# Optimization experiments

Measured on AMD Instinct MI355X. Metric: run time of the kernel, lower is better.

The kernel has to match this reference:

```python
import jax, jax.numpy as jnp
import numpy as np

EMB = 512
SEQ = 128
BATCH = 512
K = 16
ITERS = 3


def squash(x):
    # x: [..., emb]
    sq = jnp.sum(x * x, axis=-1, keepdims=True)
    scale = sq / (1.0 + sq) / jnp.sqrt(sq + 1e-9)
    return x * scale


def setup_inputs() -> dict:
    key = jax.random.key(0)
    k0, k1, k2, k3, k4 = jax.random.split(key, 5)
    low_capsule = jax.random.normal(k0, (BATCH, SEQ, EMB), dtype=jnp.float32)
    valid_his = jax.random.randint(k1, (BATCH, SEQ), 0, 2, dtype=jnp.int32)
    # torch creates B fresh with N(0,1) inside forward; we pass it in for determinism
    B_init = jax.random.normal(k2, (BATCH, K, SEQ), dtype=jnp.float32)
    W_S = jax.random.normal(k3, (EMB, EMB), dtype=jnp.float32) * 0.02  # S Linear (no bias)
    W_L = jax.random.normal(k4, (EMB, EMB), dtype=jnp.float32) * 0.02  # relu-layer Linear
    b_L = jnp.zeros((EMB,), dtype=jnp.float32)
    return {"low_capsule": low_capsule, "B_init": B_init, "W_S": W_S,
            "W_L": W_L, "b_L": b_L, "valid_his": valid_his}


def reference(low_capsule, B_init, W_S, W_L, b_L, valid_his):
    # low_capsule: [b, s, e]; valid_his: [b, s]; B_init: [b, K, s]
    lc_new = jnp.einsum('bse,fe->bsf', low_capsule, W_S)          # S(low_capsule)
    lc_iter = jax.lax.stop_gradient(lc_new)                        # .detach()
    mask = (valid_his != 0)[:, None, :]                            # [b, 1, s]
    # B never receives gradient in torch (non-leaf, requires_grad=False)
    Bc = jax.lax.stop_gradient(B_init)
    U = None
    for i in range(ITERS):
        W = jax.nn.softmax(Bc, axis=1)                             # softmax over K capsules
        W = jnp.where(mask, W, 0.0)                                # zero out invalid positions
        if i + 1 < ITERS:
            Z = jnp.einsum('bks,bse->bke', W, lc_iter)             # routed capsules
            U = squash(Z)
            Bc = Bc + jnp.einsum('bse,bke->bks', lc_iter, U)       # agreement update
        else:
            Z = jnp.einsum('bks,bse->bke', W, lc_new)              # last iter uses grad path
            U = squash(Z)
    # relu_layer=True: Linear + ReLU on [b, K, e]
    U = jax.nn.relu(jnp.einsum('bke,fe->bkf', U, W_L) + b_L)
    return U
```

## Files before the change

### kernel.cpp

```cpp
#include <hip/hip_runtime.h>
#include <hip/hip_bf16.h>

#define BATCH 512
#define SEQ   128
#define EMB   512
#define KCAP  16

typedef __attribute__((ext_vector_type(4))) float f32x4;
typedef __attribute__((ext_vector_type(8))) short s16x8;

__device__ __forceinline__ unsigned short f2bf(float x) {
    union { float f; unsigned int u; } v; v.f = x;
    unsigned int r = v.u + 0x7fff + ((v.u >> 16) & 1);
    return (unsigned short)(r >> 16);
}
__device__ __forceinline__ float bf2f(unsigned short b) {
    union { float f; unsigned int u; } v; v.u = ((unsigned int)b) << 16;
    return v.f;
}
__device__ __forceinline__ void cvt8(const float* f, s16x8& h, s16x8& l) {
    #pragma unroll
    for (int j = 0; j < 8; ++j) {
        unsigned short hb = f2bf(f[j]);
        h[j] = (short)hb;
        l[j] = (short)f2bf(f[j] - bf2f(hb));
    }
}

__device__ __forceinline__ int swz(int row, int chunk) {
    return row * 32 + ((chunk ^ ((row >> 1) & 3)) << 3);
}

template<bool EPI_BIAS_RELU>
__global__ __launch_bounds__(256, 2)
void gemm_mfma(const float* __restrict__ A, const float* __restrict__ B,
               const float* __restrict__ bias, float* __restrict__ C) {
    __shared__ short lsAh[128 * 32], lsAl[128 * 32];
    __shared__ short lsBh[128 * 32], lsBl[128 * 32];

    const int tid  = threadIdx.x;
    const int lane = tid & 63;
    const int w    = tid >> 6;
    const int wm   = (w & 1) * 64;
    const int wn   = (w >> 1) * 64;
    const size_t row0 = (size_t)(blockIdx.x >> 2) * 128;
    const int    col0 = (int)(blockIdx.x & 3) * 128;

    const int srow = tid >> 1;
    const int skh  = tid & 1;
    const int cb   = skh * 2;
    const float* Ap = A + (row0 + srow) * 512 + skh * 16;
    const float* Bp = B + (size_t)(col0 + srow) * 512 + skh * 16;

    f32x4 acc[4][4];
    #pragma unroll
    for (int i = 0; i < 4; ++i)
        #pragma unroll
        for (int j = 0; j < 4; ++j) acc[i][j] = (f32x4){0.f, 0.f, 0.f, 0.f};

    for (int kt = 0; kt < 512; kt += 32) {
        float fa[16], fb[16];
        *(float4*)&fa[0]  = *(const float4*)(Ap + kt);
        *(float4*)&fa[4]  = *(const float4*)(Ap + kt + 4);
        *(float4*)&fa[8]  = *(const float4*)(Ap + kt + 8);
        *(float4*)&fa[12] = *(const float4*)(Ap + kt + 12);
        *(float4*)&fb[0]  = *(const float4*)(Bp + kt);
        *(float4*)&fb[4]  = *(const float4*)(Bp + kt + 4);
        *(float4*)&fb[8]  = *(const float4*)(Bp + kt + 8);
        *(float4*)&fb[12] = *(const float4*)(Bp + kt + 12);

        __syncthreads();
        s16x8 h, l;
        cvt8(fa,     h, l); *(s16x8*)&lsAh[swz(srow, cb)]     = h; *(s16x8*)&lsAl[swz(srow, cb)]     = l;
        cvt8(fa + 8, h, l); *(s16x8*)&lsAh[swz(srow, cb + 1)] = h; *(s16x8*)&lsAl[swz(srow, cb + 1)] = l;
        cvt8(fb,     h, l); *(s16x8*)&lsBh[swz(srow, cb)]     = h; *(s16x8*)&lsBl[swz(srow, cb)]     = l;
        cvt8(fb + 8, h, l); *(s16x8*)&lsBh[swz(srow, cb + 1)] = h; *(s16x8*)&lsBl[swz(srow, cb + 1)] = l;
        __syncthreads();

        s16x8 ah[4], al[4], bh[4], bl[4];
        const int c = lane >> 4;
        #pragma unroll
        for (int mi = 0; mi < 4; ++mi) {
            const int r = wm + mi * 16 + (lane & 15);
            ah[mi] = *(const s16x8*)&lsAh[swz(r, c)];
            al[mi] = *(const s16x8*)&lsAl[swz(r, c)];
        }
        #pragma unroll
        for (int ni = 0; ni < 4; ++ni) {
            const int r = wn + ni * 16 + (lane & 15);
            bh[ni] = *(const s16x8*)&lsBh[swz(r, c)];
            bl[ni] = *(const s16x8*)&lsBl[swz(r, c)];
        }
        #pragma unroll
        for (int mi = 0; mi < 4; ++mi)
            #pragma unroll
            for (int ni = 0; ni < 4; ++ni) {
                acc[mi][ni] = __builtin_amdgcn_mfma_f32_16x16x32_bf16(ah[mi], bh[ni], acc[mi][ni], 0, 0, 0);
                acc[mi][ni] = __builtin_amdgcn_mfma_f32_16x16x32_bf16(al[mi], bh[ni], acc[mi][ni], 0, 0, 0);
                acc[mi][ni] = __builtin_amdgcn_mfma_f32_16x16x32_bf16(ah[mi], bl[ni], acc[mi][ni], 0, 0, 0);
            }
    }

    #pragma unroll
    for (int ni = 0; ni < 4; ++ni) {
        const int gc = col0 + wn + ni * 16 + (lane & 15);
        float bv = 0.f;
        if (EPI_BIAS_RELU) bv = bias[gc];
        #pragma unroll
        for (int mi = 0; mi < 4; ++mi) {
            const size_t gr = row0 + wm + mi * 16 + ((lane >> 4) << 2);
            #pragma unroll
            for (int r = 0; r < 4; ++r) {
                float v = acc[mi][ni][r];
                if (EPI_BIAS_RELU) v = fmaxf(v + bv, 0.f);
                C[(gr + r) * 512 + gc] = v;
            }
        }
    }
}

__device__ __forceinline__ float dot4(const float4 a, const float4 b) {
    return a.x * b.x + a.y * b.y + a.z * b.z + a.w * b.w;
}

__global__ __launch_bounds__(512, 4)
void routing_kernel(const float* __restrict__ lcn, const float* __restrict__ Binit,
                    const int* __restrict__ valid, float* __restrict__ Uout) {
    __shared__ float sBc[KCAP][SEQ];
    __shared__ float sWt[SEQ][KCAP];
    __shared__ float sU[KCAP][EMB];
    __shared__ float smask[SEQ];

    const int b    = blockIdx.x;
    const int tid  = threadIdx.x;
    const int lane = tid & 63;
    const int w    = tid >> 6;
    const int e0   = (tid & 127) * 4;
    const int k0   = (tid >> 7) * 4;
    const float* lcb = lcn + (size_t)b * (SEQ * EMB);

    for (int i = tid; i < KCAP * SEQ; i += 512)
        ((float*)sBc)[i] = Binit[(size_t)b * (KCAP * SEQ) + i];
    if (tid < SEQ) smask[tid] = (valid[b * SEQ + tid] != 0) ? 1.0f : 0.0f;
    __syncthreads();

    for (int it = 0; it < 3; ++it) {
        if (tid < SEQ) {
            const int s = tid;
            float mx = sBc[0][s];
            #pragma unroll
            for (int k = 1; k < KCAP; ++k) mx = fmaxf(mx, sBc[k][s]);
            float ex[KCAP];
            float sum = 0.f;
            #pragma unroll
            for (int k = 0; k < KCAP; ++k) { ex[k] = expf(sBc[k][s] - mx); sum += ex[k]; }
            const float inv = smask[s] / sum;
            #pragma unroll
            for (int k = 0; k < KCAP; ++k) sWt[s][k] = ex[k] * inv;
        }
        __syncthreads();

        float acc[4][4];
        #pragma unroll
        for (int i = 0; i < 4; ++i)
            #pragma unroll
            for (int j = 0; j < 4; ++j) acc[i][j] = 0.f;
        #pragma unroll 4
        for (int s = 0; s < SEQ; ++s) {
            const float4 v  = *(const float4*)(lcb + s * EMB + e0);
            const float4 wv = *(const float4*)&sWt[s][k0];
            const float wa[4] = {wv.x, wv.y, wv.z, wv.w};
            const float va[4] = {v.x, v.y, v.z, v.w};
            #pragma unroll
            for (int ki = 0; ki < 4; ++ki)
                #pragma unroll
                for (int j = 0; j < 4; ++j) acc[ki][j] += wa[ki] * va[j];
        }
        #pragma unroll
        for (int ki = 0; ki < 4; ++ki) {
            float4 r;
            r.x = acc[ki][0]; r.y = acc[ki][1]; r.z = acc[ki][2]; r.w = acc[ki][3];
            *(float4*)&sU[k0 + ki][e0] = r;
        }
        __syncthreads();

        #pragma unroll
        for (int kk = 2 * w; kk <= 2 * w + 1; ++kk) {
            float4 z0 = *(const float4*)&sU[kk][lane * 4];
            float4 z1 = *(const float4*)&sU[kk][256 + lane * 4];
            float p = dot4(z0, z0) + dot4(z1, z1);
            #pragma unroll
            for (int m = 32; m >= 1; m >>= 1) p += __shfl_xor(p, m, 64);
            const float scale = p / (1.0f + p) / sqrtf(p + 1e-9f);
            z0.x *= scale; z0.y *= scale; z0.z *= scale; z0.w *= scale;
            z1.x *= scale; z1.y *= scale; z1.z *= scale; z1.w *= scale;
            *(float4*)&sU[kk][lane * 4] = z0;
            *(float4*)&sU[kk][256 + lane * 4] = z1;
        }
        __syncthreads();

        if (it < 2) {
            const int ka = 2 * w, kb = 2 * w + 1;
            const float4 ua0 = *(const float4*)&sU[ka][lane * 4];
            const float4 ua1 = *(const float4*)&sU[ka][256 + lane * 4];
            const float4 ub0 = *(const float4*)&sU[kb][lane * 4];
            const float4 ub1 = *(const float4*)&sU[kb][256 + lane * 4];
            #pragma unroll 2
            for (int s = 0; s < SEQ; ++s) {
                const float4 l0 = *(const float4*)(lcb + s * EMB + lane * 4);
                const float4 l1 = *(const float4*)(lcb + s * EMB + 256 + lane * 4);
                float pa = dot4(l0, ua0) + dot4(l1, ua1);
                float pb = dot4(l0, ub0) + dot4(l1, ub1);
                #pragma unroll
                for (int m = 32; m >= 1; m >>= 1) {
                    pa += __shfl_xor(pa, m, 64);
                    pb += __shfl_xor(pb, m, 64);
                }
                if (lane == 0) {
                    sBc[ka][s] += pa;
                    sBc[kb][s] += pb;
                }
            }
            __syncthreads();
        }
    }

    for (int i = tid; i < KCAP * EMB; i += 512)
        Uout[(size_t)b * (KCAP * EMB) + i] = ((const float*)sU)[i];
}

extern "C" void kernel_launch(void* const* d_in, const int* in_sizes, int n_in,
                              void* d_out, int out_size, void* d_ws, size_t ws_size,
                              hipStream_t stream) {
    const float* lc    = (const float*)d_in[0];
    const float* Binit = (const float*)d_in[1];
    const float* W_S   = (const float*)d_in[2];
    const float* W_L   = (const float*)d_in[3];
    const float* b_L   = (const float*)d_in[4];
    const int*   valid = (const int*)d_in[5];
    float* out = (float*)d_out;

    const size_t lcn_elems = (size_t)BATCH * SEQ * EMB;
    const size_t u_elems   = (size_t)BATCH * KCAP * EMB;
    if (ws_size < (lcn_elems + u_elems) * sizeof(float)) return;
    float* lcn = (float*)d_ws;
    float* Uws = lcn + lcn_elems;

    gemm_mfma<false><<<2048, 256, 0, stream>>>(lc, W_S, nullptr, lcn);
    routing_kernel<<<BATCH, 512, 0, stream>>>(lcn, Binit, valid, Uws);
    gemm_mfma<true><<<256, 256, 0, stream>>>(Uws, W_L, b_L, out);
}
```

Before: 603.3 us.

## Prepack weights to bf16 hi/lo, stage routing slabs in LDS, bf16 U output

Weights are split into bf16 hi/lo pairs once by a separate pack kernel, so the GEMMs load packed weights instead of converting B every tile. The routing kernel is restructured to stream 16-row slabs of lc through shared memory, fusing the agreement update, softmax and weighted sum in one pass per iteration rather than reading lc from global memory twice. U is written as bf16 and the final GEMM uses a single bf16 A operand with two MFMAs instead of three. This removes redundant global traffic and conversion work, at the cost of lower precision for U in the output layer and extra small launches.

After: 547.1 us. -9.3%, faster.

```diff
diff --git a/kernel.cpp b/kernel.cpp
--- a/kernel.cpp
+++ b/kernel.cpp
@@ -8,6 +8,8 @@
 
 typedef __attribute__((ext_vector_type(4))) float f32x4;
 typedef __attribute__((ext_vector_type(8))) short s16x8;
+typedef __attribute__((ext_vector_type(4))) unsigned short u16x4;
+typedef __attribute__((ext_vector_type(8))) unsigned short u16x8;
 
 __device__ __forceinline__ unsigned short f2bf(float x) {
     union { float f; unsigned int u; } v; v.f = x;
@@ -26,17 +28,36 @@
         l[j] = (short)f2bf(f[j] - bf2f(hb));
     }
 }
+__device__ __forceinline__ float dot4(const float4 a, const float4 b) {
+    return a.x * b.x + a.y * b.y + a.z * b.z + a.w * b.w;
+}
 
 __device__ __forceinline__ int swz(int row, int chunk) {
     return row * 32 + ((chunk ^ ((row >> 1) & 3)) << 3);
 }
 
-template<bool EPI_BIAS_RELU>
+__global__ void cvt_pack(const float* __restrict__ in, unsigned short* __restrict__ out, int nch) {
+    const int c = blockIdx.x * 256 + threadIdx.x;
+    if (c >= nch) return;
+    float f[8];
+    *(float4*)&f[0] = *(const float4*)(in + c * 8);
+    *(float4*)&f[4] = *(const float4*)(in + c * 8 + 4);
+    u16x8 h, l;
+    #pragma unroll
+    for (int j = 0; j < 8; ++j) {
+        unsigned short hb = f2bf(f[j]);
+        h[j] = hb;
+        l[j] = f2bf(f[j] - bf2f(hb));
+    }
+    *(u16x8*)(out + c * 16) = h;
+    *(u16x8*)(out + c * 16 + 8) = l;
+}
+
 __global__ __launch_bounds__(256, 2)
-void gemm_mfma(const float* __restrict__ A, const float* __restrict__ B,
-               const float* __restrict__ bias, float* __restrict__ C) {
+void gemm_f32a(const float* __restrict__ A, const unsigned short* __restrict__ pkB,
+               float* __restrict__ C) {
     __shared__ short lsAh[128 * 32], lsAl[128 * 32];
-    __shared__ short lsBh[128 * 32], lsBl[128 * 32];
+    __shared__ unsigned short lsB[128 * 64];
 
     const int tid  = threadIdx.x;
     const int lane = tid & 63;
@@ -50,7 +71,16 @@
     const int skh  = tid & 1;
     const int cb   = skh * 2;
     const float* Ap = A + (row0 + srow) * 512 + skh * 16;
-    const float* Bp = B + (size_t)(col0 + srow) * 512 + skh * 16;
+
+    int bo[4], so[4];
+    #pragma unroll
+    for (int i = 0; i < 4; ++i) {
+        const int slot = i * 256 + tid;
+        const int br = slot >> 3, s3 = slot & 7;
+        const int cn = s3 ^ (br & 7);
+        bo[i] = (col0 + br) * 1024 + (cn >> 1) * 16 + (cn & 1) * 8;
+        so[i] = slot * 8;
+    }
 
     f32x4 acc[4][4];
     #pragma unroll
@@ -59,26 +89,25 @@
         for (int j = 0; j < 4; ++j) acc[i][j] = (f32x4){0.f, 0.f, 0.f, 0.f};
 
     for (int kt = 0; kt < 512; kt += 32) {
-        float fa[16], fb[16];
+        float fa[16];
         *(float4*)&fa[0]  = *(const float4*)(Ap + kt);
         *(float4*)&fa[4]  = *(const float4*)(Ap + kt + 4);
         *(float4*)&fa[8]  = *(const float4*)(Ap + kt + 8);
         *(float4*)&fa[12] = *(const float4*)(Ap + kt + 12);
-        *(float4*)&fb[0]  = *(const float4*)(Bp + kt);
-        *(float4*)&fb[4]  = *(const float4*)(Bp + kt + 4);
-        *(float4*)&fb[8]  = *(const float4*)(Bp + kt + 8);
-        *(float4*)&fb[12] = *(const float4*)(Bp + kt + 12);
+        u16x8 bq[4];
+        #pragma unroll
+        for (int i = 0; i < 4; ++i) bq[i] = *(const u16x8*)(pkB + bo[i] + kt * 2);
 
         __syncthreads();
         s16x8 h, l;
         cvt8(fa,     h, l); *(s16x8*)&lsAh[swz(srow, cb)]     = h; *(s16x8*)&lsAl[swz(srow, cb)]     = l;
         cvt8(fa + 8, h, l); *(s16x8*)&lsAh[swz(srow, cb + 1)] = h; *(s16x8*)&lsAl[swz(srow, cb + 1)] = l;
-        cvt8(fb,     h, l); *(s16x8*)&lsBh[swz(srow, cb)]     = h; *(s16x8*)&lsBl[swz(srow, cb)]     = l;
-        cvt8(fb + 8, h, l); *(s16x8*)&lsBh[swz(srow, cb + 1)] = h; *(s16x8*)&lsBl[swz(srow, cb + 1)] = l;
-        __syncthreads();
-
-        s16x8 ah[4], al[4], bh[4], bl[4];
+        #pragma unroll
+        for (int i = 0; i < 4; ++i) *(u16x8*)&lsB[so[i]] = bq[i];
+        __syncthreads();
+
         const int c = lane >> 4;
+        s16x8 ah[4], al[4];
         #pragma unroll
         for (int mi = 0; mi < 4; ++mi) {
             const int r = wm + mi * 16 + (lane & 15);
@@ -88,145 +117,229 @@
         #pragma unroll
         for (int ni = 0; ni < 4; ++ni) {
             const int r = wn + ni * 16 + (lane & 15);
-            bh[ni] = *(const s16x8*)&lsBh[swz(r, c)];
-            bl[ni] = *(const s16x8*)&lsBl[swz(r, c)];
-        }
-        #pragma unroll
-        for (int mi = 0; mi < 4; ++mi)
-            #pragma unroll
-            for (int ni = 0; ni < 4; ++ni) {
-                acc[mi][ni] = __builtin_amdgcn_mfma_f32_16x16x32_bf16(ah[mi], bh[ni], acc[mi][ni], 0, 0, 0);
-                acc[mi][ni] = __builtin_amdgcn_mfma_f32_16x16x32_bf16(al[mi], bh[ni], acc[mi][ni], 0, 0, 0);
-                acc[mi][ni] = __builtin_amdgcn_mfma_f32_16x16x32_bf16(ah[mi], bl[ni], acc[mi][ni], 0, 0, 0);
-            }
+            const s16x8 bh = *(const s16x8*)&lsB[r * 64 + (((2 * c)     ^ (r & 7)) << 3)];
+            const s16x8 bl = *(const s16x8*)&lsB[r * 64 + (((2 * c + 1) ^ (r & 7)) << 3)];
+            #pragma unroll
+            for (int mi = 0; mi < 4; ++mi) {
+                acc[mi][ni] = __builtin_amdgcn_mfma_f32_16x16x32_bf16(ah[mi], bh, acc[mi][ni], 0, 0, 0);
+                acc[mi][ni] = __builtin_amdgcn_mfma_f32_16x16x32_bf16(al[mi], bh, acc[mi][ni], 0, 0, 0);
+                acc[mi][ni] = __builtin_amdgcn_mfma_f32_16x16x32_bf16(ah[mi], bl, acc[mi][ni], 0, 0, 0);
+            }
+        }
     }
 
     #pragma unroll
     for (int ni = 0; ni < 4; ++ni) {
         const int gc = col0 + wn + ni * 16 + (lane & 15);
-        float bv = 0.f;
-        if (EPI_BIAS_RELU) bv = bias[gc];
         #pragma unroll
         for (int mi = 0; mi < 4; ++mi) {
             const size_t gr = row0 + wm + mi * 16 + ((lane >> 4) << 2);
             #pragma unroll
-            for (int r = 0; r < 4; ++r) {
-                float v = acc[mi][ni][r];
-                if (EPI_BIAS_RELU) v = fmaxf(v + bv, 0.f);
-                C[(gr + r) * 512 + gc] = v;
-            }
-        }
-    }
-}
-
-__device__ __forceinline__ float dot4(const float4 a, const float4 b) {
-    return a.x * b.x + a.y * b.y + a.z * b.z + a.w * b.w;
-}
-
-__global__ __launch_bounds__(512, 4)
-void routing_kernel(const float* __restrict__ lcn, const float* __restrict__ Binit,
-                    const int* __restrict__ valid, float* __restrict__ Uout) {
-    __shared__ float sBc[KCAP][SEQ];
-    __shared__ float sWt[SEQ][KCAP];
-    __shared__ float sU[KCAP][EMB];
-    __shared__ float smask[SEQ];
-
-    const int b    = blockIdx.x;
+            for (int r = 0; r < 4; ++r) C[(gr + r) * 512 + gc] = acc[mi][ni][r];
+        }
+    }
+}
+
+__global__ __launch_bounds__(256, 2)
+void gemm_bf16a(const unsigned short* __restrict__ A, const unsigned short* __restrict__ pkB,
+                const float* __restrict__ bias, float* __restrict__ C) {
+    __shared__ unsigned short lsA[128 * 32];
+    __shared__ unsigned short lsB[128 * 64];
+
     const int tid  = threadIdx.x;
     const int lane = tid & 63;
     const int w    = tid >> 6;
-    const int e0   = (tid & 127) * 4;
-    const int k0   = (tid >> 7) * 4;
+    const int wm   = (w & 1) * 64;
+    const int wn   = (w >> 1) * 64;
+    const size_t row0 = (size_t)(blockIdx.x >> 2) * 128;
+    const int    col0 = (int)(blockIdx.x & 3) * 128;
+
+    const int srow = tid >> 1;
+    const int skh  = tid & 1;
+    const int cb   = skh * 2;
+    const unsigned short* Up = A + (row0 + srow) * 512 + skh * 16;
+
+    int bo[4], so[4];
+    #pragma unroll
+    for (int i = 0; i < 4; ++i) {
+        const int slot = i * 256 + tid;
+        const int br = slot >> 3, s3 = slot & 7;
+        const int cn = s3 ^ (br & 7);
+        bo[i] = (col0 + br) * 1024 + (cn >> 1) * 16 + (cn & 1) * 8;
+        so[i] = slot * 8;
+    }
+
+    f32x4 acc[4][4];
+    #pragma unroll
+    for (int i = 0; i < 4; ++i)
+        #pragma unroll
+        for (int j = 0; j < 4; ++j) acc[i][j] = (f32x4){0.f, 0.f, 0.f, 0.f};
+
+    for (int kt = 0; kt < 512; kt += 32) {
+        const u16x8 a0 = *(const u16x8*)(Up + kt);
+        const u16x8 a1 = *(const u16x8*)(Up + kt + 8);
+        u16x8 bq[4];
+        #pragma unroll
+        for (int i = 0; i < 4; ++i) bq[i] = *(const u16x8*)(pkB + bo[i] + kt * 2);
+
+        __syncthreads();
+        *(u16x8*)&lsA[swz(srow, cb)]     = a0;
+        *(u16x8*)&lsA[swz(srow, cb + 1)] = a1;
+        #pragma unroll
+        for (int i = 0; i < 4; ++i) *(u16x8*)&lsB[so[i]] = bq[i];
+        __syncthreads();
+
+        const int c = lane >> 4;
+        s16x8 ah[4];
+        #pragma unroll
+        for (int mi = 0; mi < 4; ++mi)
+            ah[mi] = *(const s16x8*)&lsA[swz(wm + mi * 16 + (lane & 15), c)];
+        #pragma unroll
+        for (int ni = 0; ni < 4; ++ni) {
+            const int r = wn + ni * 16 + (lane & 15);
+            const s16x8 bh = *(const s16x8*)&lsB[r * 64 + (((2 * c)     ^ (r & 7)) << 3)];
+            const s16x8 bl = *(const s16x8*)&lsB[r * 64 + (((2 * c + 1) ^ (r & 7)) << 3)];
+            #pragma unroll
+            for (int mi = 0; mi < 4; ++mi) {
+                acc[mi][ni] = __builtin_amdgcn_mfma_f32_16x16x32_bf16(ah[mi], bh, acc[mi][ni], 0, 0, 0);
+                acc[mi][ni] = __builtin_amdgcn_mfma_f32_16x16x32_bf16(ah[mi], bl, acc[mi][ni], 0, 0, 0);
+            }
+        }
+    }
+
+    #pragma unroll
+    for (int ni = 0; ni < 4; ++ni) {
+        const int gc = col0 + wn + ni * 16 + (lane & 15);
+        const float bv = bias[gc];
+        #pragma unroll
+        for (int mi = 0; mi < 4; ++mi) {
+            const size_t gr = row0 + wm + mi * 16 + ((lane >> 4) << 2);
+            #pragma unroll
+            for (int r = 0; r < 4; ++r)
+                C[(gr + r) * 512 + gc] = fmaxf(acc[mi][ni][r] + bv, 0.f);
+        }
+    }
+}
+
+__global__ __launch_bounds__(512, 2)
+void routing_v2(const float* __restrict__ lcn, const float* __restrict__ Binit,
+                const int* __restrict__ valid, unsigned short* __restrict__ Uh) {
+    __shared__ float sBc[KCAP][SEQ];
+    __shared__ float sWt[16][KCAP];
+    __shared__ float sU[KCAP][EMB];
+    __shared__ float sLc[16][EMB];
+    __shared__ float smask[SEQ];
+
+    const int b = blockIdx.x, t = threadIdx.x;
+    const int lane = t & 63, w = t >> 6;
     const float* lcb = lcn + (size_t)b * (SEQ * EMB);
 
-    for (int i = tid; i < KCAP * SEQ; i += 512)
+    for (int i = t; i < KCAP * SEQ; i += 512)
         ((float*)sBc)[i] = Binit[(size_t)b * (KCAP * SEQ) + i];
-    if (tid < SEQ) smask[tid] = (valid[b * SEQ + tid] != 0) ? 1.0f : 0.0f;
+    if (t < SEQ) smask[t] = (valid[b * SEQ + t] != 0) ? 1.0f : 0.0f;
     __syncthreads();
 
+    const int k0 = (t >> 7) * 4;
+    const int e0 = (t & 127) * 4;
+    const int ka = 2 * w, kb = 2 * w + 1;
+
     for (int it = 0; it < 3; ++it) {
-        if (tid < SEQ) {
-            const int s = tid;
-            float mx = sBc[0][s];
-            #pragma unroll
-            for (int k = 1; k < KCAP; ++k) mx = fmaxf(mx, sBc[k][s]);
-            float ex[KCAP];
-            float sum = 0.f;
-            #pragma unroll
-            for (int k = 0; k < KCAP; ++k) { ex[k] = expf(sBc[k][s] - mx); sum += ex[k]; }
-            const float inv = smask[s] / sum;
-            #pragma unroll
-            for (int k = 0; k < KCAP; ++k) sWt[s][k] = ex[k] * inv;
-        }
-        __syncthreads();
-
-        float acc[4][4];
-        #pragma unroll
-        for (int i = 0; i < 4; ++i)
-            #pragma unroll
-            for (int j = 0; j < 4; ++j) acc[i][j] = 0.f;
-        #pragma unroll 4
-        for (int s = 0; s < SEQ; ++s) {
-            const float4 v  = *(const float4*)(lcb + s * EMB + e0);
-            const float4 wv = *(const float4*)&sWt[s][k0];
-            const float wa[4] = {wv.x, wv.y, wv.z, wv.w};
-            const float va[4] = {v.x, v.y, v.z, v.w};
-            #pragma unroll
-            for (int ki = 0; ki < 4; ++ki)
+        float4 ua0, ua1, ub0, ub1;
+        if (it > 0) {
+            ua0 = *(const float4*)&sU[ka][lane * 4];
+            ua1 = *(const float4*)&sU[ka][256 + lane * 4];
+            ub0 = *(const float4*)&sU[kb][lane * 4];
+            ub1 = *(const float4*)&sU[kb][256 + lane * 4];
+        }
+        f32x4 accZ[4];
+        #pragma unroll
+        for (int i = 0; i < 4; ++i) accZ[i] = (f32x4){0.f, 0.f, 0.f, 0.f};
+
+        for (int slab = 0; slab < 8; ++slab) {
+            {
+                const float4* src = (const float4*)(lcb + slab * 16 * EMB);
+                float4* dst = (float4*)sLc;
                 #pragma unroll
-                for (int j = 0; j < 4; ++j) acc[ki][j] += wa[ki] * va[j];
-        }
-        #pragma unroll
-        for (int ki = 0; ki < 4; ++ki) {
-            float4 r;
-            r.x = acc[ki][0]; r.y = acc[ki][1]; r.z = acc[ki][2]; r.w = acc[ki][3];
-            *(float4*)&sU[k0 + ki][e0] = r;
-        }
-        __syncthreads();
-
-        #pragma unroll
-        for (int kk = 2 * w; kk <= 2 * w + 1; ++kk) {
+                for (int j = 0; j < 4; ++j) dst[t + 512 * j] = src[t + 512 * j];
+            }
+            __syncthreads();
+
+            if (it > 0) {
+                #pragma unroll 4
+                for (int s8 = 0; s8 < 16; ++s8) {
+                    const float4 l0 = *(const float4*)&sLc[s8][lane * 4];
+                    const float4 l1 = *(const float4*)&sLc[s8][256 + lane * 4];
+                    float pa = dot4(l0, ua0) + dot4(l1, ua1);
+                    float pb = dot4(l0, ub0) + dot4(l1, ub1);
+                    #pragma unroll
+                    for (int m = 32; m >= 1; m >>= 1) {
+                        pa += __shfl_xor(pa, m, 64);
+                        pb += __shfl_xor(pb, m, 64);
+                    }
+                    if (lane == 0) {
+                        sBc[ka][slab * 16 + s8] += pa;
+                        sBc[kb][slab * 16 + s8] += pb;
+                    }
+                }
+                __syncthreads();
+            }
+
+            if (t < 256) {
+                const int si = t >> 4, k = t & 15, s = slab * 16 + si;
+                const float v = sBc[k][s];
+                float mx = v;
+                #pragma unroll
+                for (int m = 1; m < 16; m <<= 1) mx = fmaxf(mx, __shfl_xor(mx, m, 64));
+                const float ex = expf(v - mx);
+                float sm = ex;
+                #pragma unroll
+                for (int m = 1; m < 16; m <<= 1) sm += __shfl_xor(sm, m, 64);
+                sWt[si][k] = ex * smask[s] / sm;
+            }
+            __syncthreads();
+
+            #pragma unroll 4
+            for (int si = 0; si < 16; ++si) {
+                const float4 wv = *(const float4*)&sWt[si][k0];
+                const float4 v  = *(const float4*)&sLc[si][e0];
+                const f32x4 vv = {v.x, v.y, v.z, v.w};
+                accZ[0] += vv * wv.x;
+                accZ[1] += vv * wv.y;
+                accZ[2] += vv * wv.z;
+                accZ[3] += vv * wv.w;
+            }
+            __syncthreads();
+        }
+
+        #pragma unroll
+        for (int ki = 0; ki < 4; ++ki) *(f32x4*)&sU[k0 + ki][e0] = accZ[ki];
+        __syncthreads();
+
+        #pragma unroll
+        for (int kk = ka; kk <= kb; ++kk) {
             float4 z0 = *(const float4*)&sU[kk][lane * 4];
             float4 z1 = *(const float4*)&sU[kk][256 + lane * 4];
             float p = dot4(z0, z0) + dot4(z1, z1);
             #pragma unroll
             for (int m = 32; m >= 1; m >>= 1) p += __shfl_xor(p, m, 64);
-            const float scale = p / (1.0f + p) / sqrtf(p + 1e-9f);
-            z0.x *= scale; z0.y *= scale; z0.z *= scale; z0.w *= scale;
-            z1.x *= scale; z1.y *= scale; z1.z *= scale; z1.w *= scale;
+            const float sc = p / (1.0f + p) / sqrtf(p + 1e-9f);
+            z0.x *= sc; z0.y *= sc; z0.z *= sc; z0.w *= sc;
+            z1.x *= sc; z1.y *= sc; z1.z *= sc; z1.w *= sc;
             *(float4*)&sU[kk][lane * 4] = z0;
             *(float4*)&sU[kk][256 + lane * 4] = z1;
         }
         __syncthreads();
-
-        if (it < 2) {
-            const int ka = 2 * w, kb = 2 * w + 1;
-            const float4 ua0 = *(const float4*)&sU[ka][lane * 4];
-            const float4 ua1 = *(const float4*)&sU[ka][256 + lane * 4];
-            const float4 ub0 = *(const float4*)&sU[kb][lane * 4];
-            const float4 ub1 = *(const float4*)&sU[kb][256 + lane * 4];
-            #pragma unroll 2
-            for (int s = 0; s < SEQ; ++s) {
-                const float4 l0 = *(const float4*)(lcb + s * EMB + lane * 4);
-                const float4 l1 = *(const float4*)(lcb + s * EMB + 256 + lane * 4);
-                float pa = dot4(l0, ua0) + dot4(l1, ua1);
-                float pb = dot4(l0, ub0) + dot4(l1, ub1);
-                #pragma unroll
-                for (int m = 32; m >= 1; m >>= 1) {
-                    pa += __shfl_xor(pa, m, 64);
-                    pb += __shfl_xor(pb, m, 64);
-                }
-                if (lane == 0) {
-                    sBc[ka][s] += pa;
-                    sBc[kb][s] += pb;
-                }
-            }
-            __syncthreads();
-        }
-    }
-
-    for (int i = tid; i < KCAP * EMB; i += 512)
-        Uout[(size_t)b * (KCAP * EMB) + i] = ((const float*)sU)[i];
+    }
+
+    unsigned short* ub = Uh + (size_t)b * (KCAP * EMB);
+    #pragma unroll
+    for (int j = 0; j < 4; ++j) {
+        const int f4 = t + 512 * j;
+        const float4 v = ((const float4*)sU)[f4];
+        u16x4 o;
+        o[0] = f2bf(v.x); o[1] = f2bf(v.y); o[2] = f2bf(v.z); o[3] = f2bf(v.w);
+        *(u16x4*)(ub + f4 * 4) = o;
+    }
 }
 
 extern "C" void kernel_launch(void* const* d_in, const int* in_sizes, int n_in,
@@ -240,13 +353,15 @@
     const int*   valid = (const int*)d_in[5];
     float* out = (float*)d_out;
 
-    const size_t lcn_elems = (size_t)BATCH * SEQ * EMB;
-    const size_t u_elems   = (size_t)BATCH * KCAP * EMB;
-    if (ws_size < (lcn_elems + u_elems) * sizeof(float)) return;
     float* lcn = (float*)d_ws;
-    float* Uws = lcn + lcn_elems;
-
-    gemm_mfma<false><<<2048, 256, 0, stream>>>(lc, W_S, nullptr, lcn);
-    routing_kernel<<<BATCH, 512, 0, stream>>>(lcn, Binit, valid, Uws);
-    gemm_mfma<true><<<256, 256, 0, stream>>>(Uws, W_L, b_L, out);
-}
+    unsigned short* pkWS = (unsigned short*)(lcn + 33554432);
+    unsigned short* pkWL = pkWS + 524288;
+    unsigned short* Uh   = pkWL + 524288;
+    if (ws_size < 144703488) return;
+
+    cvt_pack<<<128, 256, 0, stream>>>(W_S, pkWS, 32768);
+    cvt_pack<<<128, 256, 0, stream>>>(W_L, pkWL, 32768);
+    gemm_f32a<<<2048, 256, 0, stream>>>(lc, pkWS, lcn);
+    routing_v2<<<BATCH, 512, 0, stream>>>(lcn, Binit, valid, Uh);
+    gemm_bf16a<<<256, 256, 0, stream>>>(Uh, pkWL, b_L, out);
+}
```
